# Optimization experiments

Measured on AMD Instinct MI355X. Metric: run time of the kernel, lower is better.

The kernel has to match this reference:

```python
import jax, jax.numpy as jnp
import numpy as np

ALPHA = 1.0
ARAP_WEIGHT = 1.0
B, N, K, LATENT, HIDDEN = 16, 20000, 16, 256, 1024


def setup_inputs() -> dict:
    key = jax.random.key(0)
    ks = jax.random.split(key, 8)
    code = jax.random.normal(ks[0], (B, LATENT), jnp.float32)
    W1 = jax.random.normal(ks[1], (LATENT, HIDDEN), jnp.float32) / np.sqrt(LATENT)
    b1 = jnp.zeros((HIDDEN,), jnp.float32)
    W2 = jax.random.normal(ks[2], (HIDDEN, N * 3), jnp.float32) / np.sqrt(HIDDEN)
    b2 = jnp.zeros((N * 3,), jnp.float32)
    xyz1 = jax.random.normal(ks[3], (B, N, 3), jnp.float32)
    weightMatrix = jax.random.uniform(ks[4], (N, K), jnp.float32)
    area = jax.random.uniform(ks[5], (N,), jnp.float32)
    neighborsMatrix = jax.random.randint(ks[6], (N, K), 0, N, jnp.int32)
    numNeighbors = jax.random.randint(ks[7], (N,), 1, K + 1, jnp.int32)
    return {"code": code, "W1": W1, "b1": b1, "W2": W2, "b2": b2,
            "xyz1": xyz1, "weightMatrix": weightMatrix, "area": area,
            "neighborsMatrix": neighborsMatrix, "numNeighbors": numNeighbors}


def _mean_energy(code, W1, b1, W2, b2, xyz1, weightMatrix, area,
                 neighborsMatrix, numNeighbors):
    # decoder: MLP latent -> hidden -> N*3, reshaped to [B,N,3]
    h = jax.nn.relu(code @ W1 + b1)
    recon = (h @ W2 + b2).reshape(B, N, 3)

    # mask out padded neighbor slots, fold into weights  [N,K]
    mask = (jnp.arange(K)[None, :] < numNeighbors[:, None]).astype(jnp.float32)
    wm = weightMatrix * mask

    # neighbor-gathered edge vectors: rest pose d, deformed dq  [B,N,K,3]
    d = xyz1[:, :, None, :] - xyz1[:, neighborsMatrix, :]
    dq = recon[:, :, None, :] - recon[:, neighborsMatrix, :]

    # per-vertex weighted covariance and best-fit rotation (Procrustes)
    S = jnp.einsum('nk,bnki,bnkj->bnij', wm, d, dq)          # [B,N,3,3]
    U, s, Vt = jnp.linalg.svd(S)
    V = jnp.swapaxes(Vt, -1, -2)
    Ut = jnp.swapaxes(U, -1, -2)
    det = jnp.linalg.det(V @ Ut)                              # [B,N]
    Vf = V.at[..., :, -1].multiply(jnp.sign(det)[..., None])  # reflection fix
    R = jax.lax.stop_gradient(Vf @ Ut)                        # R treated as constant

    resid = dq - jnp.einsum('bnij,bnkj->bnki', R, d)          # [B,N,K,3]
    e = (ARAP_WEIGHT * ALPHA) * area[None, :, None] * wm[None] \
        * jnp.sum(resid * resid, axis=-1)                     # [B,N,K]
    # torch.mean(torch.mean(e, 2), 1)
    return jnp.mean(e, axis=(1, 2))                           # [B]


def reference(code, W1, b1, W2, b2, xyz1, weightMatrix, area,
              neighborsMatrix, numNeighbors):
    meanEnergy = _mean_energy(code, W1, b1, W2, b2, xyz1, weightMatrix, area,
                              neighborsMatrix, numNeighbors)
    # meanEnergy.backward(ones) -> grad of sum(meanEnergy) wrt code
    code_grad = jax.grad(lambda c: jnp.sum(
        _mean_energy(c, W1, b1, W2, b2, xyz1, weightMatrix, area,
                     neighborsMatrix, numNeighbors)))(code)
    return (meanEnergy, code_grad)
```

## Files before the change

kernel.cpp:

```cpp
#include <hip/hip_runtime.h>

constexpr int B_ = 16;
constexpr int NV = 20000;
constexpr int KN = 16;
constexpr int LAT = 256;
constexpr int HID = 1024;
constexpr int N3 = 60000;
constexpr int RCAP = 64;
constexpr int NCHUNK = 8;
constexpr float INV_NK = 1.0f / (20000.0f * 16.0f);

constexpr size_t H_OFF      = 0;
constexpr size_t XYZT_OFF   = H_OFF + B_ * HID;
constexpr size_t RECONT_OFF = XYZT_OFF + (size_t)N3 * 16;
constexpr size_t GRECON_OFF = RECONT_OFF + (size_t)N3 * 16;
constexpr size_t GH_OFF     = GRECON_OFF + (size_t)B_ * N3;
constexpr size_t RBUF_OFF   = GH_OFF + B_ * HID;
constexpr size_t RCOUNT_OFF = RBUF_OFF + (size_t)NV * 12 * 16;
constexpr size_t RLIST_OFF  = RCOUNT_OFF + NV;
constexpr size_t PART_OFF   = RLIST_OFF + (size_t)NV * RCAP;

__device__ __forceinline__ void atomAddF(float* p, float v) {
  unsafeAtomicAdd(p, v);
}

__global__ __launch_bounds__(256) void k_mlp1(
    const float* __restrict__ code, const float* __restrict__ W1,
    const float* __restrict__ b1, float* __restrict__ h) {
  int t = blockIdx.x * 256 + threadIdx.x;
  int b = t >> 10, hd = t & 1023;
  const float* c = code + b * LAT;
  float acc = b1[hd];
  #pragma unroll 4
  for (int l = 0; l < LAT; ++l) acc += c[l] * W1[l * HID + hd];
  h[t] = fmaxf(acc, 0.0f);
}

__global__ __launch_bounds__(256) void k_xpose(
    const float* __restrict__ xyz, float* __restrict__ xyzT) {
  __shared__ float sm[64][17];
  const int tid = threadIdx.x;
  const int n30 = blockIdx.x * 64;
  {
    const int n3l = tid & 63, bq = tid >> 6;
    #pragma unroll
    for (int p = 0; p < 4; ++p) {
      int b = p * 4 + bq;
      if (n30 + n3l < N3) sm[n3l][b] = xyz[(size_t)b * N3 + n30 + n3l];
    }
  }
  __syncthreads();
  {
    const int b = tid & 15, nq = tid >> 4;
    #pragma unroll
    for (int p = 0; p < 4; ++p) {
      int n3l = p * 16 + nq;
      if (n30 + n3l < N3) xyzT[(size_t)(n30 + n3l) * 16 + b] = sm[n3l][b];
    }
  }
}

__global__ __launch_bounds__(256) void k_mlp2(
    const float* __restrict__ h, const float* __restrict__ W2,
    float* __restrict__ part) {
  __shared__ float hs[16][128];
  const int tid = threadIdx.x;
  const int hd0 = blockIdx.y * 128;
  #pragma unroll
  for (int r = 0; r < 8; ++r) {
    int idx = r * 256 + tid;
    int bb = idx >> 7, cc = idx & 127;
    hs[bb][cc] = h[bb * HID + hd0 + cc];
  }
  __syncthreads();

  const int j4 = blockIdx.x * 1024 + tid * 4;
  if (j4 >= N3) return;

  float4 acc[16];
  #pragma unroll
  for (int b = 0; b < 16; ++b) acc[b] = make_float4(0.f, 0.f, 0.f, 0.f);

  const float* wp = W2 + (size_t)hd0 * N3 + j4;
  float4 w0 = *(const float4*)(wp);
  float4 w1 = *(const float4*)(wp + (size_t)N3);
  float4 w2 = *(const float4*)(wp + (size_t)2 * N3);
  float4 w3 = *(const float4*)(wp + (size_t)3 * N3);

  for (int g = 0; g < 32; ++g) {
    const float* np = wp + (size_t)4 * N3;
    float4 n0, n1, n2, n3;
    if (g < 31) {
      n0 = *(const float4*)(np);
      n1 = *(const float4*)(np + (size_t)N3);
      n2 = *(const float4*)(np + (size_t)2 * N3);
      n3 = *(const float4*)(np + (size_t)3 * N3);
    }
    #pragma unroll
    for (int b = 0; b < 16; ++b) {
      float4 hb = *(const float4*)&hs[b][g * 4];
      acc[b].x += hb.x * w0.x + hb.y * w1.x + hb.z * w2.x + hb.w * w3.x;
      acc[b].y += hb.x * w0.y + hb.y * w1.y + hb.z * w2.y + hb.w * w3.y;
      acc[b].z += hb.x * w0.z + hb.y * w1.z + hb.z * w2.z + hb.w * w3.z;
      acc[b].w += hb.x * w0.w + hb.y * w1.w + hb.z * w2.w + hb.w * w3.w;
    }
    wp = np; w0 = n0; w1 = n1; w2 = n2; w3 = n3;
  }

  float ac[4][16];
  #pragma unroll
  for (int b = 0; b < 16; ++b) {
    ac[0][b] = acc[b].x; ac[1][b] = acc[b].y;
    ac[2][b] = acc[b].z; ac[3][b] = acc[b].w;
  }
  float* pbase = part + ((size_t)blockIdx.y * N3 + j4) * 16;
  #pragma unroll
  for (int jj = 0; jj < 4; ++jj)
    #pragma unroll
    for (int q = 0; q < 4; ++q)
      *(float4*)(pbase + jj * 16 + q * 4) = make_float4(
          ac[jj][q*4+0], ac[jj][q*4+1], ac[jj][q*4+2], ac[jj][q*4+3]);
}

__global__ __launch_bounds__(256) void k_reduce(
    const float* __restrict__ part, const float* __restrict__ b2,
    float* __restrict__ reconT) {
  int t = blockIdx.x * 256 + threadIdx.x;
  if (t >= N3 * 16 / 4) return;
  size_t pos = (size_t)t * 4;
  int j = t >> 2;
  float4 s = *(const float4*)(part + pos);
  #pragma unroll
  for (int c = 1; c < NCHUNK; ++c) {
    float4 p = *(const float4*)(part + (size_t)c * N3 * 16 + pos);
    s.x += p.x; s.y += p.y; s.z += p.z; s.w += p.w;
  }
  float bias = b2[j];
  s.x += bias; s.y += bias; s.z += bias; s.w += bias;
  *(float4*)(reconT + pos) = s;
}

__global__ __launch_bounds__(256) void k_fill(
    const int* __restrict__ nbrs, const int* __restrict__ nnbr,
    int* __restrict__ rcount, int* __restrict__ rlist) {
  int e = blockIdx.x * 256 + threadIdx.x;
  int n = e >> 4, k = e & 15;
  if (k < nnbr[n]) {
    int v = nbrs[e];
    int slot = atomicAdd(&rcount[v], 1);
    if (slot < RCAP) rlist[v * RCAP + slot] = e;
  }
}

__global__ __launch_bounds__(256, 2) void k_rot(
    const float* __restrict__ xT, const float* __restrict__ qT,
    const float* __restrict__ wmat, const float* __restrict__ area,
    const int* __restrict__ nbrs, const int* __restrict__ nnbr,
    float* __restrict__ Rbuf, float* __restrict__ energy) {
  __shared__ float red[64];
  const int tid = threadIdx.x;
  const int b = tid & 15, nl = tid >> 4;
  const int n = blockIdx.x * 16 + nl;
  const int nn = nnbr[n];
  const float ar = area[n];
  const float x0 = xT[(size_t)n*48 + b],      x1 = xT[(size_t)n*48 + 16 + b],
              x2 = xT[(size_t)n*48 + 32 + b];
  const float q0 = qT[(size_t)n*48 + b],      q1 = qT[(size_t)n*48 + 16 + b],
              q2 = qT[(size_t)n*48 + 32 + b];

  float dX[KN], dY[KN], dZ[KN], eX[KN], eY[KN], eZ[KN], wk[KN];
  float S00=0,S01=0,S02=0,S10=0,S11=0,S12=0,S20=0,S21=0,S22=0;
  #pragma unroll
  for (int k = 0; k < KN; ++k) {
    float w=0, dx=0, dy=0, dz=0, ex=0, ey=0, ez=0;
    if (k < nn) {
      int m = nbrs[n * KN + k];
      w = wmat[n * KN + k];
      size_t mb = (size_t)m * 48 + b;
      dx = x0 - xT[mb]; dy = x1 - xT[mb + 16]; dz = x2 - xT[mb + 32];
      ex = q0 - qT[mb]; ey = q1 - qT[mb + 16]; ez = q2 - qT[mb + 32];
    }
    wk[k]=w; dX[k]=dx; dY[k]=dy; dZ[k]=dz; eX[k]=ex; eY[k]=ey; eZ[k]=ez;
    S00 += w*dx*ex; S01 += w*dx*ey; S02 += w*dx*ez;
    S10 += w*dy*ex; S11 += w*dy*ey; S12 += w*dy*ez;
    S20 += w*dz*ex; S21 += w*dz*ey; S22 += w*dz*ez;
  }

  float A00 = S00*S00 + S10*S10 + S20*S20;
  float A01 = S00*S01 + S10*S11 + S20*S21;
  float A02 = S00*S02 + S10*S12 + S20*S22;
  float A11 = S01*S01 + S11*S11 + S21*S21;
  float A12 = S01*S02 + S11*S12 + S21*S22;
  float A22 = S02*S02 + S12*S12 + S22*S22;
  float V00=1,V01=0,V02=0, V10=0,V11=1,V12=0, V20=0,V21=0,V22=1;

  auto rot = [&](float& app, float& aqq, float& apq, float& arp, float& arq,
                 float& vp0, float& vp1, float& vp2,
                 float& vq0, float& vq1, float& vq2) {
    float a = apq;
    if (fabsf(a) > 1e-37f) {
      float tau = (aqq - app) * 0.5f / a;
      float t = copysignf(1.0f, tau) / (fabsf(tau) + sqrtf(1.0f + tau * tau));
      float c = rsqrtf(1.0f + t * t);
      float s = t * c;
      float napp = c*c*app - 2.0f*s*c*a + s*s*aqq;
      float naqq = s*s*app + 2.0f*s*c*a + c*c*aqq;
      app = napp; aqq = naqq; apq = 0.0f;
      float rp = arp, rq = arq;
      arp = c*rp - s*rq; arq = s*rp + c*rq;
      float t0, t1;
      t0=vp0; t1=vq0; vp0 = c*t0 - s*t1; vq0 = s*t0 + c*t1;
      t0=vp1; t1=vq1; vp1 = c*t0 - s*t1; vq1 = s*t0 + c*t1;
      t0=vp2; t1=vq2; vp2 = c*t0 - s*t1; vq2 = s*t0 + c*t1;
    }
  };
  #pragma unroll
  for (int sweep = 0; sweep < 6; ++sweep) {
    rot(A00,A11,A01, A02,A12, V00,V10,V20, V01,V11,V21);
    rot(A00,A22,A02, A01,A12, V00,V10,V20, V02,V12,V22);
    rot(A11,A22,A12, A01,A02, V01,V11,V21, V02,V12,V22);
  }
  auto sw = [](float& a, float& c) { float t = a; a = c; c = t; };
  if (A00 < A11) { sw(A00,A11); sw(V00,V01); sw(V10,V11); sw(V20,V21); }
  if (A00 < A22) { sw(A00,A22); sw(V00,V02); sw(V10,V12); sw(V20,V22); }
  if (A11 < A22) { sw(A11,A22); sw(V01,V02); sw(V11,V12); sw(V21,V22); }

  float v1x=V00, v1y=V10, v1z=V20;
  float v2x=V01, v2y=V11, v2z=V21;

  float u1x = S00*v1x + S01*v1y + S02*v1z;
  float u1y = S10*v1x + S11*v1y + S12*v1z;
  float u1z = S20*v1x + S21*v1y + S22*v1z;
  float s1sq = u1x*u1x + u1y*u1y + u1z*u1z;
  if (s1sq > 1e-30f) { float r = rsqrtf(s1sq); u1x*=r; u1y*=r; u1z*=r; }
  else { u1x = 1.0f; u1y = 0.0f; u1z = 0.0f; }

  float u2x = S00*v2x + S01*v2y + S02*v2z;
  float u2y = S10*v2x + S11*v2y + S12*v2z;
  float u2z = S20*v2x + S21*v2y + S22*v2z;
  float pr = u2x*u1x + u2y*u1y + u2z*u1z;
  u2x -= pr*u1x; u2y -= pr*u1y; u2z -= pr*u1z;
  float s2sq = u2x*u2x + u2y*u2y + u2z*u2z;
  if (s2sq > 1e-12f * s1sq + 1e-30f) {
    float r = rsqrtf(s2sq); u2x*=r; u2y*=r; u2z*=r;
  } else {
    float ex_ = (fabsf(u1x) < 0.9f) ? 1.0f : 0.0f;
    float ey_ = 1.0f - ex_;
    float pp = ex_*u1x + ey_*u1y;
    u2x = ex_ - pp*u1x; u2y = ey_ - pp*u1y; u2z = -pp*u1z;
    float r = rsqrtf(u2x*u2x + u2y*u2y + u2z*u2z);
    u2x*=r; u2y*=r; u2z*=r;
  }
  float u3x = u1y*u2z - u1z*u2y, u3y = u1z*u2x - u1x*u2z, u3z = u1x*u2y - u1y*u2x;
  float v3x = v1y*v2z - v1z*v2y, v3y = v1z*v2x - v1x*v2z, v3z = v1x*v2y - v1y*v2x;

  float R00 = v1x*u1x + v2x*u2x + v3x*u3x;
  float R01 = v1x*u1y + v2x*u2y + v3x*u3y;
  float R02 = v1x*u1z + v2x*u2z + v3x*u3z;
  float R10 = v1y*u1x + v2y*u2x + v3y*u3x;
  float R11 = v1y*u1y + v2y*u2y + v3y*u3y;
  float R12 = v1y*u1z + v2y*u2z + v3y*u3z;
  float R20 = v1z*u1x + v2z*u2x + v3z*u3x;
  float R21 = v1z*u1y + v2z*u2y + v3z*u3y;
  float R22 = v1z*u1z + v2z*u2z + v3z*u3z;

  float esum = 0, go0 = 0, go1 = 0, go2 = 0;
  const float gf = 2.0f * ar * INV_NK;
  #pragma unroll
  for (int k = 0; k < KN; ++k) {
    float w = wk[k];
    float dx = dX[k], dy = dY[k], dz = dZ[k];
    float rx = eX[k] - (R00*dx + R01*dy + R02*dz);
    float ry = eY[k] - (R10*dx + R11*dy + R12*dz);
    float rz = eZ[k] - (R20*dx + R21*dy + R22*dz);
    esum += w * (rx*rx + ry*ry + rz*rz);
    float gc = gf * w;
    go0 += gc*rx; go1 += gc*ry; go2 += gc*rz;
  }
  esum *= ar * INV_NK;

  float* rb = Rbuf + (size_t)n * 192 + b;
  rb[0]=R00;  rb[16]=R01;  rb[32]=R02;
  rb[48]=R10; rb[64]=R11;  rb[80]=R12;
  rb[96]=R20; rb[112]=R21; rb[128]=R22;
  rb[144]=go0; rb[160]=go1; rb[176]=go2;

  esum += __shfl_down(esum, 32);
  esum += __shfl_down(esum, 16);
  int wave = tid >> 6, lane = tid & 63;
  if (lane < 16) red[wave * 16 + lane] = esum;
  __syncthreads();
  if (tid < 16) atomAddF(&energy[tid], red[tid] + red[16 + tid] + red[32 + tid] + red[48 + tid]);
}

__global__ __launch_bounds__(256) void k_scatter(
    const float* __restrict__ xT, const float* __restrict__ qT,
    const float* __restrict__ wmat, const float* __restrict__ area,
    const float* __restrict__ Rbuf, const int* __restrict__ rcount,
    const int* __restrict__ rlist, float* __restrict__ grecon) {
  int t = blockIdx.x * 256 + threadIdx.x;
  int v = t >> 4, b = t & 15;
  const float xv0 = xT[(size_t)v*48 + b], xv1 = xT[(size_t)v*48 + 16 + b],
              xv2 = xT[(size_t)v*48 + 32 + b];
  const float qv0 = qT[(size_t)v*48 + b], qv1 = qT[(size_t)v*48 + 16 + b],
              qv2 = qT[(size_t)v*48 + 32 + b];
  float g0 = 0, g1 = 0, g2 = 0;
  int deg = min(rcount[v], RCAP);
  for (int i = 0; i < deg; ++i) {
    int e = rlist[v * RCAP + i];
    int n = e >> 4;
    float gc = 2.0f * INV_NK * area[n] * wmat[e];
    const float* rb = Rbuf + (size_t)n * 192 + b;
    size_t nb = (size_t)n * 48 + b;
    float dx = xT[nb] - xv0, dy = xT[nb+16] - xv1, dz = xT[nb+32] - xv2;
    float ex = qT[nb] - qv0, ey = qT[nb+16] - qv1, ez = qT[nb+32] - qv2;
    float rx = ex - (rb[0]*dx  + rb[16]*dy  + rb[32]*dz);
    float ry = ey - (rb[48]*dx + rb[64]*dy  + rb[80]*dz);
    float rz = ez - (rb[96]*dx + rb[112]*dy + rb[128]*dz);
    g0 -= gc*rx; g1 -= gc*ry; g2 -= gc*rz;
  }
  const float* ob = Rbuf + (size_t)v * 192 + b;
  g0 += ob[144]; g1 += ob[160]; g2 += ob[176];
  float* gq = grecon + (size_t)b * N3 + v * 3;
  gq[0] = g0; gq[1] = g1; gq[2] = g2;
}

__global__ __launch_bounds__(256, 2) void k_mlp2_bwd(
    const float* __restrict__ gr, const float* __restrict__ W2,
    float* __restrict__ gh) {
  const int tid = threadIdx.x;
  const int lane = tid & 63;
  const int wv = tid >> 6;
  const int laneJ = lane & 15, laneR = lane >> 4;
  const int row0 = blockIdx.y * 32 + wv * 8 + laneR * 2;

  float4 acc0[16], acc1[16];
  #pragma unroll
  for (int b = 0; b < 16; ++b) {
    acc0[b] = make_float4(0.f, 0.f, 0.f, 0.f);
    acc1[b] = make_float4(0.f, 0.f, 0.f, 0.f);
  }

  const int jbase = blockIdx.x * 64 + laneJ * 4;
  const float* w2r0 = W2 + (size_t)row0 * N3;
  const float* w2r1 = W2 + (size_t)(row0 + 1) * N3;

  for (int it = 0; it < 59; ++it) {
    int j = jbase + it * 1024;
    if (j < N3) {
      float4 w0 = *(const float4*)(w2r0 + j);
      float4 w1 = *(const float4*)(w2r1 + j);
      #pragma unroll
      for (int b = 0; b < 16; ++b) {
        float4 g = *(const float4*)(gr + (size_t)b * N3 + j);
        acc0[b].x += g.x * w0.x; acc0[b].y += g.y * w0.y;
        acc0[b].z += g.z * w0.z; acc0[b].w += g.w * w0.w;
        acc1[b].x += g.x * w1.x; acc1[b].y += g.y * w1.y;
        acc1[b].z += g.z * w1.z; acc1[b].w += g.w * w1.w;
      }
    }
  }

  float s0[16], s1[16];
  #pragma unroll
  for (int b = 0; b < 16; ++b) {
    s0[b] = (acc0[b].x + acc0[b].y) + (acc0[b].z + acc0[b].w);
    s1[b] = (acc1[b].x + acc1[b].y) + (acc1[b].z + acc1[b].w);
  }
  #pragma unroll
  for (int m = 1; m <= 8; m <<= 1) {
    #pragma unroll
    for (int b = 0; b < 16; ++b) {
      s0[b] += __shfl_xor(s0[b], m);
      s1[b] += __shfl_xor(s1[b], m);
    }
  }
  if (laneJ == 0) {
    #pragma unroll
    for (int b = 0; b < 16; ++b) {
      atomAddF(&gh[b * HID + row0], s0[b]);
      atomAddF(&gh[b * HID + row0 + 1], s1[b]);
    }
  }
}

__global__ __launch_bounds__(256) void k_mlp1_bwd(
    const float* __restrict__ gh, const float* __restrict__ h,
    const float* __restrict__ W1, float* __restrict__ gcode) {
  __shared__ float gm[128];
  const int b = blockIdx.x;
  const int hd0 = blockIdx.y * 128;
  const int l = threadIdx.x;
  if (l < 128) {
    float g = gh[b * HID + hd0 + l];
    gm[l] = (h[b * HID + hd0 + l] > 0.0f) ? g : 0.0f;
  }
  __syncthreads();
  const float4* wp = (const float4*)(W1 + (size_t)l * HID + hd0);
  float acc = 0.0f;
  #pragma unroll
  for (int i = 0; i < 32; ++i) {
    float4 w4 = wp[i];
    acc += w4.x * gm[i*4+0] + w4.y * gm[i*4+1] + w4.z * gm[i*4+2] + w4.w * gm[i*4+3];
  }
  atomAddF(&gcode[b * LAT + l], acc);
}

extern "C" void kernel_launch(void* const* d_in, const int* in_sizes, int n_in,
                              void* d_out, int out_size, void* d_ws, size_t ws_size,
                              hipStream_t stream) {
  const float* code = (const float*)d_in[0];
  const float* W1   = (const float*)d_in[1];
  const float* b1   = (const float*)d_in[2];
  const float* W2   = (const float*)d_in[3];
  const float* b2   = (const float*)d_in[4];
  const float* xyz  = (const float*)d_in[5];
  const float* wmat = (const float*)d_in[6];
  const float* area = (const float*)d_in[7];
  const int* nbrs   = (const int*)d_in[8];
  const int* nnbr   = (const int*)d_in[9];

  float* out = (float*)d_out;
  float* ws = (float*)d_ws;
  float* h      = ws + H_OFF;
  float* xyzT   = ws + XYZT_OFF;
  float* reconT = ws + RECONT_OFF;
  float* grecon = ws + GRECON_OFF;
  float* gh     = ws + GH_OFF;
  float* Rbuf   = ws + RBUF_OFF;
  int*   rcount = (int*)(ws + RCOUNT_OFF);
  int*   rlist  = (int*)(ws + RLIST_OFF);
  float* part   = ws + PART_OFF;

  hipMemsetAsync(gh, 0, (size_t)B_ * HID * sizeof(float), stream);
  hipMemsetAsync(rcount, 0, (size_t)NV * sizeof(int), stream);
  hipMemsetAsync(out, 0, (size_t)(B_ + B_ * LAT) * sizeof(float), stream);

  k_fill<<<dim3(NV * KN / 256), dim3(256), 0, stream>>>(nbrs, nnbr, rcount, rlist);
  k_xpose<<<dim3((N3 + 63) / 64), dim3(256), 0, stream>>>(xyz, xyzT);
  k_mlp1<<<dim3(64), dim3(256), 0, stream>>>(code, W1, b1, h);
  k_mlp2<<<dim3(59, NCHUNK), dim3(256), 0, stream>>>(h, W2, part);
  k_reduce<<<dim3((N3 * 16 / 4 + 255) / 256), dim3(256), 0, stream>>>(part, b2, reconT);
  k_rot<<<dim3(NV / 16), dim3(256), 0, stream>>>(
      xyzT, reconT, wmat, area, nbrs, nnbr, Rbuf, out);
  k_scatter<<<dim3(NV * 16 / 256), dim3(256), 0, stream>>>(
      xyzT, reconT, wmat, area, Rbuf, rcount, rlist, grecon);
  k_mlp2_bwd<<<dim3(16, 32), dim3(256), 0, stream>>>(grecon, W2, gh);
  k_mlp1_bwd<<<dim3(B_, 8), dim3(256), 0, stream>>>(gh, h, W1, out + B_);
}
```

Measured before the change: 599.1 us.

## Store per-edge gradients in k_rot and sum them in k_scatter

k_rot now writes the per-edge gradient contribution (gc*residual) for each valid neighbor into a new [N,K,3,B] buffer, plus the per-vertex own gradient, instead of storing the rotation matrix. k_scatter then only gathers and sums those precomputed edge gradients, no longer re-gathering xyz, recon, R, area and weights or recomputing the residual. The cost is roughly 61 MB of extra writes from k_rot against far fewer scattered reads and less arithmetic in the scatter. The scatter loop is also unrolled by two.

```diff
diff --git a/kernel.cpp b/kernel.cpp
--- a/kernel.cpp
+++ b/kernel.cpp
@@ -15,8 +15,9 @@
 constexpr size_t RECONT_OFF = XYZT_OFF + (size_t)N3 * 16;
 constexpr size_t GRECON_OFF = RECONT_OFF + (size_t)N3 * 16;
 constexpr size_t GH_OFF     = GRECON_OFF + (size_t)B_ * N3;
-constexpr size_t RBUF_OFF   = GH_OFF + B_ * HID;
-constexpr size_t RCOUNT_OFF = RBUF_OFF + (size_t)NV * 12 * 16;
+constexpr size_t OWNG_OFF   = GH_OFF + B_ * HID;
+constexpr size_t GEDGE_OFF  = OWNG_OFF + (size_t)NV * 48;
+constexpr size_t RCOUNT_OFF = GEDGE_OFF + (size_t)NV * KN * 48;
 constexpr size_t RLIST_OFF  = RCOUNT_OFF + NV;
 constexpr size_t PART_OFF   = RLIST_OFF + (size_t)NV * RCAP;
 
@@ -156,7 +157,8 @@
     const float* __restrict__ xT, const float* __restrict__ qT,
     const float* __restrict__ wmat, const float* __restrict__ area,
     const int* __restrict__ nbrs, const int* __restrict__ nnbr,
-    float* __restrict__ Rbuf, float* __restrict__ energy) {
+    float* __restrict__ ownG, float* __restrict__ gEdge,
+    float* __restrict__ energy) {
   __shared__ float red[64];
   const int tid = threadIdx.x;
   const int b = tid & 15, nl = tid >> 4;
@@ -266,6 +268,7 @@
 
   float esum = 0, go0 = 0, go1 = 0, go2 = 0;
   const float gf = 2.0f * ar * INV_NK;
+  float* geb = gEdge + (size_t)n * 768 + b;
   #pragma unroll
   for (int k = 0; k < KN; ++k) {
     float w = wk[k];
@@ -275,15 +278,17 @@
     float rz = eZ[k] - (R20*dx + R21*dy + R22*dz);
     esum += w * (rx*rx + ry*ry + rz*rz);
     float gc = gf * w;
-    go0 += gc*rx; go1 += gc*ry; go2 += gc*rz;
+    float gx = gc*rx, gy = gc*ry, gz = gc*rz;
+    go0 += gx; go1 += gy; go2 += gz;
+    if (k < nn) {
+      float* gp = geb + k * 48;
+      gp[0] = gx; gp[16] = gy; gp[32] = gz;
+    }
   }
   esum *= ar * INV_NK;
 
-  float* rb = Rbuf + (size_t)n * 192 + b;
-  rb[0]=R00;  rb[16]=R01;  rb[32]=R02;
-  rb[48]=R10; rb[64]=R11;  rb[80]=R12;
-  rb[96]=R20; rb[112]=R21; rb[128]=R22;
-  rb[144]=go0; rb[160]=go1; rb[176]=go2;
+  float* og = ownG + (size_t)n * 48 + b;
+  og[0] = go0; og[16] = go1; og[32] = go2;
 
   esum += __shfl_down(esum, 32);
   esum += __shfl_down(esum, 16);
@@ -294,33 +299,29 @@
 }
 
 __global__ __launch_bounds__(256) void k_scatter(
-    const float* __restrict__ xT, const float* __restrict__ qT,
-    const float* __restrict__ wmat, const float* __restrict__ area,
-    const float* __restrict__ Rbuf, const int* __restrict__ rcount,
-    const int* __restrict__ rlist, float* __restrict__ grecon) {
+    const float* __restrict__ gEdge, const float* __restrict__ ownG,
+    const int* __restrict__ rcount, const int* __restrict__ rlist,
+    float* __restrict__ grecon) {
   int t = blockIdx.x * 256 + threadIdx.x;
   int v = t >> 4, b = t & 15;
-  const float xv0 = xT[(size_t)v*48 + b], xv1 = xT[(size_t)v*48 + 16 + b],
-              xv2 = xT[(size_t)v*48 + 32 + b];
-  const float qv0 = qT[(size_t)v*48 + b], qv1 = qT[(size_t)v*48 + 16 + b],
-              qv2 = qT[(size_t)v*48 + 32 + b];
-  float g0 = 0, g1 = 0, g2 = 0;
+  const float* og = ownG + (size_t)v * 48 + b;
+  float g0 = og[0], g1 = og[16], g2 = og[32];
   int deg = min(rcount[v], RCAP);
-  for (int i = 0; i < deg; ++i) {
-    int e = rlist[v * RCAP + i];
-    int n = e >> 4;
-    float gc = 2.0f * INV_NK * area[n] * wmat[e];
-    const float* rb = Rbuf + (size_t)n * 192 + b;
-    size_t nb = (size_t)n * 48 + b;
-    float dx = xT[nb] - xv0, dy = xT[nb+16] - xv1, dz = xT[nb+32] - xv2;
-    float ex = qT[nb] - qv0, ey = qT[nb+16] - qv1, ez = qT[nb+32] - qv2;
-    float rx = ex - (rb[0]*dx  + rb[16]*dy  + rb[32]*dz);
-    float ry = ey - (rb[48]*dx + rb[64]*dy  + rb[80]*dz);
-    float rz = ez - (rb[96]*dx + rb[112]*dy + rb[128]*dz);
-    g0 -= gc*rx; g1 -= gc*ry; g2 -= gc*rz;
-  }
-  const float* ob = Rbuf + (size_t)v * 192 + b;
-  g0 += ob[144]; g1 += ob[160]; g2 += ob[176];
+  const int* rl = rlist + v * RCAP;
+  int i = 0;
+  for (; i + 1 < deg; i += 2) {
+    int e0 = rl[i], e1 = rl[i + 1];
+    const float* p0 = gEdge + (size_t)e0 * 48 + b;
+    const float* p1 = gEdge + (size_t)e1 * 48 + b;
+    g0 -= p0[0]  + p1[0];
+    g1 -= p0[16] + p1[16];
+    g2 -= p0[32] + p1[32];
+  }
+  if (i < deg) {
+    int e = rl[i];
+    const float* p = gEdge + (size_t)e * 48 + b;
+    g0 -= p[0]; g1 -= p[16]; g2 -= p[32];
+  }
   float* gq = grecon + (size_t)b * N3 + v * 3;
   gq[0] = g0; gq[1] = g1; gq[2] = g2;
 }
@@ -427,7 +428,8 @@
   float* reconT = ws + RECONT_OFF;
   float* grecon = ws + GRECON_OFF;
   float* gh     = ws + GH_OFF;
-  float* Rbuf   = ws + RBUF_OFF;
+  float* ownG   = ws + OWNG_OFF;
+  float* gEdge  = ws + GEDGE_OFF;
   int*   rcount = (int*)(ws + RCOUNT_OFF);
   int*   rlist  = (int*)(ws + RLIST_OFF);
   float* part   = ws + PART_OFF;
@@ -442,9 +444,9 @@
   k_mlp2<<<dim3(59, NCHUNK), dim3(256), 0, stream>>>(h, W2, part);
   k_reduce<<<dim3((N3 * 16 / 4 + 255) / 256), dim3(256), 0, stream>>>(part, b2, reconT);
   k_rot<<<dim3(NV / 16), dim3(256), 0, stream>>>(
-      xyzT, reconT, wmat, area, nbrs, nnbr, Rbuf, out);
+      xyzT, reconT, wmat, area, nbrs, nnbr, ownG, gEdge, out);
   k_scatter<<<dim3(NV * 16 / 256), dim3(256), 0, stream>>>(
-      xyzT, reconT, wmat, area, Rbuf, rcount, rlist, grecon);
+      gEdge, ownG, rcount, rlist, grecon);
   k_mlp2_bwd<<<dim3(16, 32), dim3(256), 0, stream>>>(grecon, W2, gh);
   k_mlp1_bwd<<<dim3(B_, 8), dim3(256), 0, stream>>>(gh, h, W1, out + B_);
 }
```

Measured after the change: 583.8 us. 1.03x faster.
